# Performance work log

Hardware: AMD Instinct MI355X
Metric: run time of the kernel (lower is better)

Reference implementation:

```python
import jax, jax.numpy as jnp
import numpy as np

N = 8192        # number of nodes (adjacency is N x N)
F_IN = 256      # in_features
F_OUT = 256     # out_features


def setup_inputs() -> dict:
    key = jax.random.key(0)
    k_x, k_adj, k_kernel, k_bias, k_beta = jax.random.split(key, 5)
    x = jax.random.normal(k_x, (N, F_IN), dtype=jnp.float32)
    adj = jax.random.uniform(k_adj, (N, N), dtype=jnp.float32)  # dense non-negative adjacency buffer
    # xavier-uniform-like scale for the kernel
    limit = float(np.sqrt(6.0 / (F_IN + F_OUT)))
    kernel = jax.random.uniform(k_kernel, (F_IN, F_OUT), dtype=jnp.float32, minval=-limit, maxval=limit)
    bias = 0.01 * jax.random.normal(k_bias, (F_OUT,), dtype=jnp.float32)
    beta = 0.01 * jax.random.normal(k_beta, (N,), dtype=jnp.float32)
    return {"x": x, "adj": adj, "kernel": kernel, "bias": bias, "beta": beta}


def reference(x, adj, kernel, bias, beta):
    # Original: diag(1/(rowsum(adj)+beta)) @ (adj + diag(beta)) @ x @ kernel + bias
    # Fused form: row-scale and diagonal-add applied without materializing NxN diag matrices.
    scale = jnp.reciprocal(jnp.sum(adj, axis=1) + beta)          # [N]
    agg = adj @ x + beta[:, None] * x                             # (adj + diag(beta)) @ x  -> [N, F_IN]
    return (scale[:, None] * agg) @ kernel + bias                 # [N, F_OUT]
```

## Files before the change

kernel.cpp:

```cpp
#include <hip/hip_runtime.h>
#include <hip/hip_bf16.h>


typedef __attribute__((ext_vector_type(8))) short  short8;
typedef __attribute__((ext_vector_type(4))) float  floatx4;

#define N_NODES 8192
#define F_DIM   256

#define ASYNC16(g, l)                                                          \
  __builtin_amdgcn_global_load_lds(                                           \
      (const __attribute__((address_space(1))) void*)(g),                     \
      (__attribute__((address_space(3))) void*)(l), 16, 0, 0)

__device__ __forceinline__ unsigned short f2bf(float f) {
  unsigned u = __float_as_uint(f);
  return (unsigned short)((u + 0x7FFFu + ((u >> 16) & 1u)) >> 16);
}

__device__ __forceinline__ short8 pack_bf16x8(floatx4 a, floatx4 b) {
  short8 r;
  r[0] = (short)f2bf(a.x);
  r[1] = (short)f2bf(a.y);
  r[2] = (short)f2bf(a.z);
  r[3] = (short)f2bf(a.w);
  r[4] = (short)f2bf(b.x);
  r[5] = (short)f2bf(b.y);
  r[6] = (short)f2bf(b.z);
  r[7] = (short)f2bf(b.w);
  return r;
}

__global__ __launch_bounds__(256) void tile_bf16_kernel(
    const float* __restrict__ src, unsigned short* __restrict__ dst, int K) {
  const int Nn = F_DIM;
  int cid = blockIdx.x * 256 + threadIdx.x;
  int per_kblk = Nn * 4;
  int kblk = cid / per_kblk;
  int rem  = cid - kblk * per_kblk;
  int n16 = rem >> 6;
  int kg  = (rem >> 4) & 3;
  int nl  = rem & 15;
  int n = n16 * 16 + nl;
  int k = kblk * 32 + kg * 8;
  const float* s = src + (size_t)k * Nn + n;
  floatx4 v0, v1;
  v0.x = s[0];
  v0.y = s[(size_t)Nn];
  v0.z = s[(size_t)2 * Nn];
  v0.w = s[(size_t)3 * Nn];
  v1.x = s[(size_t)4 * Nn];
  v1.y = s[(size_t)5 * Nn];
  v1.z = s[(size_t)6 * Nn];
  v1.w = s[(size_t)7 * Nn];
  *(short8*)(dst + (size_t)cid * 8) = pack_bf16x8(v0, v1);
}

template <int KS>
__global__ __launch_bounds__(256, 2) void stage1_kernel(
    const float* __restrict__ adj, const unsigned short* __restrict__ xbt,
    float* __restrict__ part, float* __restrict__ rsp) {
  __shared__ float         At[64 * 32];
  __shared__ unsigned short Bt[32 * F_DIM];

  const int tid = threadIdx.x;
  const int w  = tid >> 6;
  const int l  = tid & 63;
  const int kq = l >> 4;
  const int ml = l & 15;
  const int m0 = blockIdx.x * 64;
  const int ks = blockIdx.y;
  const int kbeg   = ks * (N_NODES / KS);
  const int KSTEPS = (N_NODES / KS) / 32;

  const int arow = w * 16 + (l >> 3);
  const int srcg = (l & 7) ^ ((l >> 3) & 7);
  const float* agp0 = adj + (size_t)(m0 + arow) * N_NODES + kbeg + srcg * 4;
  const float* agp1 = agp0 + (size_t)8 * N_NODES;
  float* aldst0 = At + (w * 2) * 256;
  float* aldst1 = At + (w * 2 + 1) * 256;
  const unsigned short* bgp =
      xbt + (size_t)(kbeg / 32) * (32 * F_DIM) + (w * 4) * 512 + l * 8;
  unsigned short* bldst = Bt + (w * 4) * 512;

  int aoff0[4], aoff1[4], boff[4];
#pragma unroll
  for (int mf = 0; mf < 4; ++mf) {
    int m = mf * 16 + ml;
    aoff0[mf] = m * 32 + (((kq * 2)     ^ (m & 7)) * 4);
    aoff1[mf] = m * 32 + (((kq * 2 + 1) ^ (m & 7)) * 4);
  }
#pragma unroll
  for (int nf = 0; nf < 4; ++nf)
    boff[nf] = (w * 4 + nf) * 512 + kq * 128 + ml * 8;

  floatx4 acc[4][4];
  const floatx4 zf4 = {0.f, 0.f, 0.f, 0.f};
#pragma unroll
  for (int mf = 0; mf < 4; ++mf)
#pragma unroll
    for (int nf = 0; nf < 4; ++nf) acc[mf][nf] = zf4;
  float rsum[4] = {0.f, 0.f, 0.f, 0.f};

  for (int s = 0; s < KSTEPS; ++s) {
    ASYNC16(agp0, aldst0);
    ASYNC16(agp1, aldst1);
    ASYNC16(bgp,         bldst);
    ASYNC16(bgp +  512,  bldst +  512);
    ASYNC16(bgp + 1024,  bldst + 1024);
    ASYNC16(bgp + 1536,  bldst + 1536);
    agp0 += 32; agp1 += 32; bgp += 32 * F_DIM;
    __syncthreads();

    short8 af[4];
#pragma unroll
    for (int mf = 0; mf < 4; ++mf) {
      floatx4 a0 = *(const floatx4*)(At + aoff0[mf]);
      floatx4 a1 = *(const floatx4*)(At + aoff1[mf]);
      if (w == 0)
        rsum[mf] += (a0.x + a0.y + a0.z + a0.w) + (a1.x + a1.y + a1.z + a1.w);
      af[mf] = pack_bf16x8(a0, a1);
    }
#pragma unroll
    for (int nf = 0; nf < 4; ++nf) {
      short8 bv = *(const short8*)(Bt + boff[nf]);
#pragma unroll
      for (int mf = 0; mf < 4; ++mf)
        acc[mf][nf] =
            __builtin_amdgcn_mfma_f32_16x16x32_bf16(af[mf], bv, acc[mf][nf], 0, 0, 0);
    }
    __syncthreads();
  }

  float* pout = part + (size_t)ks * N_NODES * F_DIM;
#pragma unroll
  for (int mf = 0; mf < 4; ++mf)
#pragma unroll
    for (int nf = 0; nf < 4; ++nf) {
      int col = w * 64 + nf * 16 + ml;
#pragma unroll
      for (int r = 0; r < 4; ++r) {
        int row = m0 + mf * 16 + kq * 4 + r;
        pout[(size_t)row * F_DIM + col] = acc[mf][nf][r];
      }
    }

  if (w == 0) {
#pragma unroll
    for (int mf = 0; mf < 4; ++mf) {
      float v = rsum[mf];
      v += __shfl_xor(v, 16);
      v += __shfl_xor(v, 32);
      if (kq == 0) rsp[ks * N_NODES + m0 + mf * 16 + ml] = v;
    }
  }
}

template <int KS>
__global__ __launch_bounds__(256, 2) void stage2_kernel(
    const float* part, const float* __restrict__ rsp,
    const float* __restrict__ x, const float* __restrict__ beta,
    const float* __restrict__ bias, const unsigned short* __restrict__ wbt,
    float* out) {
  __shared__ unsigned short At[32 * 32];
  __shared__ unsigned short Bt[32 * F_DIM];
  __shared__ float sscale[32];
  __shared__ float sbeta[32];

  const int tid = threadIdx.x;
  const int w  = tid >> 6;
  const int l  = tid & 63;
  const int kq = l >> 4;
  const int ml = l & 15;
  const int m0 = blockIdx.x * 32;

  if (tid < 32) {
    float rs = 0.f;
#pragma unroll
    for (int p = 0; p < KS; ++p) rs += rsp[p * N_NODES + m0 + tid];
    float b = beta[m0 + tid];
    sbeta[tid]  = b;
    sscale[tid] = 1.0f / (rs + b);
  }
  __syncthreads();

  floatx4 acc[2][4];
  const floatx4 zf4 = {0.f, 0.f, 0.f, 0.f};
#pragma unroll
  for (int mf = 0; mf < 2; ++mf)
#pragma unroll
    for (int nf = 0; nf < 4; ++nf) acc[mf][nf] = zf4;

  const unsigned short* bgp = wbt + (w * 4) * 512 + l * 8;
  unsigned short* bldst = Bt + (w * 4) * 512;

  for (int s = 0; s < 8; ++s) {
    ASYNC16(bgp,        bldst);
    ASYNC16(bgp +  512, bldst +  512);
    ASYNC16(bgp + 1024, bldst + 1024);
    ASYNC16(bgp + 1536, bldst + 1536);
    bgp += 32 * F_DIM;

    if (tid < 128) {
      int r = tid >> 2, g = tid & 3;
      size_t off = (size_t)(m0 + r) * F_DIM + s * 32 + g * 8;
      floatx4 v0 = *(const floatx4*)(x + off);
      floatx4 v1 = *(const floatx4*)(x + off + 4);
      float bb = sbeta[r];
      v0 *= bb; v1 *= bb;
#pragma unroll
      for (int p = 0; p < KS; ++p) {
        const float* pp = part + (size_t)p * N_NODES * F_DIM + off;
        v0 += *(const floatx4*)pp;
        v1 += *(const floatx4*)(pp + 4);
      }
      float sc = sscale[r];
      v0 *= sc; v1 *= sc;
      *(short8*)(At + r * 32 + ((g ^ (r & 3)) * 8)) = pack_bf16x8(v0, v1);
    }
    __syncthreads();

    short8 af[2];
#pragma unroll
    for (int mf = 0; mf < 2; ++mf) {
      int m = mf * 16 + ml;
      af[mf] = *(const short8*)(At + m * 32 + ((kq ^ (m & 3)) * 8));
    }
#pragma unroll
    for (int nf = 0; nf < 4; ++nf) {
      short8 bv = *(const short8*)(Bt + (w * 4 + nf) * 512 + kq * 128 + ml * 8);
#pragma unroll
      for (int mf = 0; mf < 2; ++mf)
        acc[mf][nf] =
            __builtin_amdgcn_mfma_f32_16x16x32_bf16(af[mf], bv, acc[mf][nf], 0, 0, 0);
    }
    __syncthreads();
  }

#pragma unroll
  for (int nf = 0; nf < 4; ++nf) {
    int col = w * 64 + nf * 16 + ml;
    float bv = bias[col];
#pragma unroll
    for (int mf = 0; mf < 2; ++mf)
#pragma unroll
      for (int r = 0; r < 4; ++r) {
        int row = m0 + mf * 16 + kq * 4 + r;
        out[(size_t)row * F_DIM + col] = acc[mf][nf][r] + bv;
      }
  }
}

extern "C" void kernel_launch(void* const* d_in, const int* in_sizes, int n_in,
                              void* d_out, int out_size, void* d_ws, size_t ws_size,
                              hipStream_t stream) {
  const float* x    = (const float*)d_in[0];
  const float* adj  = (const float*)d_in[1];
  const float* kern = (const float*)d_in[2];
  const float* bias = (const float*)d_in[3];
  const float* beta = (const float*)d_in[4];
  float* out = (float*)d_out;

  char* ws = (char*)d_ws;
  unsigned short* xbt = (unsigned short*)ws;
  unsigned short* wbt = xbt + (size_t)N_NODES * F_DIM;
  float* rsp  = (float*)(wbt + F_DIM * F_DIM);
  float* part = (float*)((char*)rsp + 4 * N_NODES * sizeof(float));

  const size_t base    = (size_t)N_NODES * F_DIM * 2 + (size_t)F_DIM * F_DIM * 2 +
                         4 * (size_t)N_NODES * 4;
  const size_t part_sz = (size_t)N_NODES * F_DIM * 4;

  tile_bf16_kernel<<<(N_NODES * F_DIM / 8) / 256, 256, 0, stream>>>(x, xbt, N_NODES);
  tile_bf16_kernel<<<(F_DIM * F_DIM / 8) / 256, 256, 0, stream>>>(kern, wbt, F_DIM);

  if (ws_size >= base + 4 * part_sz) {
    stage1_kernel<4><<<dim3(128, 4), 256, 0, stream>>>(adj, xbt, part, rsp);
    stage2_kernel<4><<<256, 256, 0, stream>>>(part, rsp, x, beta, bias, wbt, out);
  } else if (ws_size >= base + 2 * part_sz) {
    stage1_kernel<2><<<dim3(128, 2), 256, 0, stream>>>(adj, xbt, part, rsp);
    stage2_kernel<2><<<256, 256, 0, stream>>>(part, rsp, x, beta, bias, wbt, out);
  } else {
    stage1_kernel<1><<<dim3(128, 1), 256, 0, stream>>>(adj, xbt, out, rsp);
    stage2_kernel<1><<<256, 256, 0, stream>>>(out, rsp, x, beta, bias, wbt, out);
  }
}
```

Before: 431.9 us.

## Fuse both GEMM stages into one kernel with a 3-stage async LDS pipeline

Replaces the split-K stage1 and the separate stage2 kernel with one fused kernel. Each 512-thread block owns 32 rows and loops over the full K. A triple-buffered global_load_lds pipeline waits on vmcnt, with BK=64. The aggregated tile is scaled, given the beta*x term, converted to bf16 in LDS and multiplied by the kernel weights in the same block. This removes the fp32 partial-sum round trip through global memory and one launch, and overlaps loads with MFMA. In exchange it uses about 123KB of LDS per block (likely one block per CU), has no split-K parallelism, and re-reads xbt once per row tile.

Result: faster. 416.9 us (-3.5%).

```diff
diff --git a/kernel.cpp b/kernel.cpp
--- a/kernel.cpp
+++ b/kernel.cpp
@@ -7,6 +7,8 @@
 
 #define N_NODES 8192
 #define F_DIM   256
+#define BK      64
+#define NSTEPS  (N_NODES / BK)
 
 #define ASYNC16(g, l)                                                          \
   __builtin_amdgcn_global_load_lds(                                           \
@@ -56,198 +58,155 @@
   *(short8*)(dst + (size_t)cid * 8) = pack_bf16x8(v0, v1);
 }
 
-template <int KS>
-__global__ __launch_bounds__(256, 2) void stage1_kernel(
+__global__ __launch_bounds__(512, 2) void fused_kernel(
     const float* __restrict__ adj, const unsigned short* __restrict__ xbt,
-    float* __restrict__ part, float* __restrict__ rsp) {
-  __shared__ float         At[64 * 32];
-  __shared__ unsigned short Bt[32 * F_DIM];
-
-  const int tid = threadIdx.x;
-  const int w  = tid >> 6;
-  const int l  = tid & 63;
-  const int kq = l >> 4;
-  const int ml = l & 15;
-  const int m0 = blockIdx.x * 64;
-  const int ks = blockIdx.y;
-  const int kbeg   = ks * (N_NODES / KS);
-  const int KSTEPS = (N_NODES / KS) / 32;
-
-  const int arow = w * 16 + (l >> 3);
-  const int srcg = (l & 7) ^ ((l >> 3) & 7);
-  const float* agp0 = adj + (size_t)(m0 + arow) * N_NODES + kbeg + srcg * 4;
-  const float* agp1 = agp0 + (size_t)8 * N_NODES;
-  float* aldst0 = At + (w * 2) * 256;
-  float* aldst1 = At + (w * 2 + 1) * 256;
-  const unsigned short* bgp =
-      xbt + (size_t)(kbeg / 32) * (32 * F_DIM) + (w * 4) * 512 + l * 8;
-  unsigned short* bldst = Bt + (w * 4) * 512;
-
-  int aoff0[4], aoff1[4], boff[4];
-#pragma unroll
-  for (int mf = 0; mf < 4; ++mf) {
-    int m = mf * 16 + ml;
-    aoff0[mf] = m * 32 + (((kq * 2)     ^ (m & 7)) * 4);
-    aoff1[mf] = m * 32 + (((kq * 2 + 1) ^ (m & 7)) * 4);
-  }
-#pragma unroll
-  for (int nf = 0; nf < 4; ++nf)
-    boff[nf] = (w * 4 + nf) * 512 + kq * 128 + ml * 8;
-
-  floatx4 acc[4][4];
-  const floatx4 zf4 = {0.f, 0.f, 0.f, 0.f};
-#pragma unroll
-  for (int mf = 0; mf < 4; ++mf)
-#pragma unroll
-    for (int nf = 0; nf < 4; ++nf) acc[mf][nf] = zf4;
-  float rsum[4] = {0.f, 0.f, 0.f, 0.f};
-
-  for (int s = 0; s < KSTEPS; ++s) {
-    ASYNC16(agp0, aldst0);
-    ASYNC16(agp1, aldst1);
-    ASYNC16(bgp,         bldst);
-    ASYNC16(bgp +  512,  bldst +  512);
-    ASYNC16(bgp + 1024,  bldst + 1024);
-    ASYNC16(bgp + 1536,  bldst + 1536);
-    agp0 += 32; agp1 += 32; bgp += 32 * F_DIM;
-    __syncthreads();
-
-    short8 af[4];
-#pragma unroll
-    for (int mf = 0; mf < 4; ++mf) {
-      floatx4 a0 = *(const floatx4*)(At + aoff0[mf]);
-      floatx4 a1 = *(const floatx4*)(At + aoff1[mf]);
-      if (w == 0)
-        rsum[mf] += (a0.x + a0.y + a0.z + a0.w) + (a1.x + a1.y + a1.z + a1.w);
-      af[mf] = pack_bf16x8(a0, a1);
-    }
-#pragma unroll
-    for (int nf = 0; nf < 4; ++nf) {
-      short8 bv = *(const short8*)(Bt + boff[nf]);
-#pragma unroll
-      for (int mf = 0; mf < 4; ++mf)
-        acc[mf][nf] =
-            __builtin_amdgcn_mfma_f32_16x16x32_bf16(af[mf], bv, acc[mf][nf], 0, 0, 0);
-    }
-    __syncthreads();
-  }
-
-  float* pout = part + (size_t)ks * N_NODES * F_DIM;
-#pragma unroll
-  for (int mf = 0; mf < 4; ++mf)
-#pragma unroll
-    for (int nf = 0; nf < 4; ++nf) {
-      int col = w * 64 + nf * 16 + ml;
-#pragma unroll
-      for (int r = 0; r < 4; ++r) {
-        int row = m0 + mf * 16 + kq * 4 + r;
-        pout[(size_t)row * F_DIM + col] = acc[mf][nf][r];
-      }
-    }
-
-  if (w == 0) {
-#pragma unroll
-    for (int mf = 0; mf < 4; ++mf) {
-      float v = rsum[mf];
-      v += __shfl_xor(v, 16);
-      v += __shfl_xor(v, 32);
-      if (kq == 0) rsp[ks * N_NODES + m0 + mf * 16 + ml] = v;
-    }
-  }
-}
-
-template <int KS>
-__global__ __launch_bounds__(256, 2) void stage2_kernel(
-    const float* part, const float* __restrict__ rsp,
     const float* __restrict__ x, const float* __restrict__ beta,
     const float* __restrict__ bias, const unsigned short* __restrict__ wbt,
-    float* out) {
-  __shared__ unsigned short At[32 * 32];
-  __shared__ unsigned short Bt[32 * F_DIM];
-  __shared__ float sscale[32];
-  __shared__ float sbeta[32];
+    float* __restrict__ out) {
+  __shared__ __attribute__((aligned(16))) char smem[123136];
+  float* sscale = (float*)(smem + 122880);
+  float* sbeta  = (float*)(smem + 123008);
 
   const int tid = threadIdx.x;
-  const int w  = tid >> 6;
-  const int l  = tid & 63;
-  const int kq = l >> 4;
-  const int ml = l & 15;
-  const int m0 = blockIdx.x * 32;
-
-  if (tid < 32) {
-    float rs = 0.f;
-#pragma unroll
-    for (int p = 0; p < KS; ++p) rs += rsp[p * N_NODES + m0 + tid];
-    float b = beta[m0 + tid];
-    sbeta[tid]  = b;
-    sscale[tid] = 1.0f / (rs + b);
-  }
+  const int w   = tid >> 6;
+  const int l   = tid & 63;
+  const int kq  = l >> 4;
+  const int ml  = l & 15;
+  const int wm  = w >> 2;
+  const int wn  = w & 3;
+  const int m0  = blockIdx.x * 32;
+
+  const int arow = tid >> 4;
+  const int agrp = tid & 15;
+  const float* asrc_base =
+      adj + (size_t)(m0 + arow) * N_NODES + ((agrp ^ (arow & 7)) << 2);
+  const unsigned short* bsrc_base = xbt + (size_t)tid * 8;
+
+  const int frow = wm * 16 + ml;
+  int aoff[2][2];
+#pragma unroll
+  for (int kb = 0; kb < 2; ++kb) {
+    int g0 = kb * 8 + kq * 2;
+    aoff[kb][0] = frow * 64 + (((g0)     ^ (frow & 7)) << 2);
+    aoff[kb][1] = frow * 64 + (((g0 + 1) ^ (frow & 7)) << 2);
+  }
+  const int boffbase = wn * 2048 + kq * 128 + ml * 8;
+
+  floatx4 acc[4];
+  const floatx4 zf4 = {0.f, 0.f, 0.f, 0.f};
+#pragma unroll
+  for (int nf = 0; nf < 4; ++nf) acc[nf] = zf4;
+  float rsum = 0.f;
+
+#pragma unroll
+  for (int s = 0; s < 2; ++s) {
+    ASYNC16(asrc_base + s * BK, smem + s * 8192 + (w << 10));
+    const unsigned short* bs = bsrc_base + (size_t)s * 16384;
+    char* bd = smem + 24576 + s * 32768 + (w << 10);
+#pragma unroll
+    for (int q = 0; q < 4; ++q) ASYNC16(bs + q * 4096, bd + q * 8192);
+  }
+
+  auto compute = [&](int cur) {
+    const float* Af = (const float*)(smem + cur * 8192);
+    const unsigned short* Bf = (const unsigned short*)(smem + 24576 + cur * 32768);
+    short8 af[2];
+#pragma unroll
+    for (int kb = 0; kb < 2; ++kb) {
+      floatx4 a0 = *(const floatx4*)(Af + aoff[kb][0]);
+      floatx4 a1 = *(const floatx4*)(Af + aoff[kb][1]);
+      if (wn == 0)
+        rsum += (a0.x + a0.y + a0.z + a0.w) + (a1.x + a1.y + a1.z + a1.w);
+      af[kb] = pack_bf16x8(a0, a1);
+    }
+#pragma unroll
+    for (int nf = 0; nf < 4; ++nf) {
+      short8 b0 = *(const short8*)(Bf + boffbase + nf * 512);
+      short8 b1 = *(const short8*)(Bf + 8192 + boffbase + nf * 512);
+      acc[nf] = __builtin_amdgcn_mfma_f32_16x16x32_bf16(af[0], b0, acc[nf], 0, 0, 0);
+      acc[nf] = __builtin_amdgcn_mfma_f32_16x16x32_bf16(af[1], b1, acc[nf], 0, 0, 0);
+    }
+  };
+
+  int cur = 0, stg = 2;
+  for (int s = 0; s < NSTEPS - 2; ++s) {
+    asm volatile("s_waitcnt vmcnt(5)\n\ts_barrier" ::: "memory");
+    ASYNC16(asrc_base + (s + 2) * BK, smem + stg * 8192 + (w << 10));
+    {
+      const unsigned short* bs = bsrc_base + (size_t)(s + 2) * 16384;
+      char* bd = smem + 24576 + stg * 32768 + (w << 10);
+#pragma unroll
+      for (int q = 0; q < 4; ++q) ASYNC16(bs + q * 4096, bd + q * 8192);
+    }
+    compute(cur);
+    cur = cur + 1; if (cur == 3) cur = 0;
+    stg = stg + 1; if (stg == 3) stg = 0;
+  }
+  for (int s = NSTEPS - 2; s < NSTEPS; ++s) {
+    asm volatile("s_waitcnt vmcnt(0)\n\ts_barrier" ::: "memory");
+    compute(cur);
+    cur = cur + 1; if (cur == 3) cur = 0;
+  }
+
   __syncthreads();
 
-  floatx4 acc[2][4];
-  const floatx4 zf4 = {0.f, 0.f, 0.f, 0.f};
-#pragma unroll
-  for (int mf = 0; mf < 2; ++mf)
-#pragma unroll
-    for (int nf = 0; nf < 4; ++nf) acc[mf][nf] = zf4;
-
-  const unsigned short* bgp = wbt + (w * 4) * 512 + l * 8;
-  unsigned short* bldst = Bt + (w * 4) * 512;
-
-  for (int s = 0; s < 8; ++s) {
-    ASYNC16(bgp,        bldst);
-    ASYNC16(bgp +  512, bldst +  512);
-    ASYNC16(bgp + 1024, bldst + 1024);
-    ASYNC16(bgp + 1536, bldst + 1536);
-    bgp += 32 * F_DIM;
-
-    if (tid < 128) {
-      int r = tid >> 2, g = tid & 3;
-      size_t off = (size_t)(m0 + r) * F_DIM + s * 32 + g * 8;
-      floatx4 v0 = *(const floatx4*)(x + off);
-      floatx4 v1 = *(const floatx4*)(x + off + 4);
-      float bb = sbeta[r];
-      v0 *= bb; v1 *= bb;
-#pragma unroll
-      for (int p = 0; p < KS; ++p) {
-        const float* pp = part + (size_t)p * N_NODES * F_DIM + off;
-        v0 += *(const floatx4*)pp;
-        v1 += *(const floatx4*)(pp + 4);
-      }
-      float sc = sscale[r];
-      v0 *= sc; v1 *= sc;
-      *(short8*)(At + r * 32 + ((g ^ (r & 3)) * 8)) = pack_bf16x8(v0, v1);
-    }
-    __syncthreads();
-
-    short8 af[2];
-#pragma unroll
-    for (int mf = 0; mf < 2; ++mf) {
-      int m = mf * 16 + ml;
-      af[mf] = *(const short8*)(At + m * 32 + ((kq ^ (m & 3)) * 8));
-    }
+  {
+    const float* xs = x + (size_t)m0 * F_DIM + tid * 4;
+    char* xd = smem + 24576 + (w << 10);
+#pragma unroll
+    for (int q = 0; q < 4; ++q) ASYNC16(xs + q * 2048, xd + q * 8192);
+  }
+  if (wn == 0) {
+    float rs = rsum;
+    rs += __shfl_xor(rs, 16);
+    rs += __shfl_xor(rs, 32);
+    if (l < 16) {
+      float b = beta[m0 + wm * 16 + l];
+      sbeta[wm * 16 + l]  = b;
+      sscale[wm * 16 + l] = 1.0f / (rs + b);
+    }
+  }
+  __syncthreads();
+
+  const float* xl = (const float*)(smem + 24576);
+  unsigned short* G = (unsigned short*)smem;
+#pragma unroll
+  for (int nf = 0; nf < 4; ++nf) {
+    int col = wn * 64 + nf * 16 + ml;
+    int chunk = col >> 3;
+#pragma unroll
+    for (int r = 0; r < 4; ++r) {
+      int row = wm * 16 + kq * 4 + r;
+      float g = sscale[row] * (acc[nf][r] + sbeta[row] * xl[row * F_DIM + col]);
+      G[row * 256 + (((chunk ^ (row & 7)) << 3) | (col & 7))] = f2bf(g);
+    }
+  }
+  __syncthreads();
+
+  floatx4 acc2[4];
+#pragma unroll
+  for (int nf = 0; nf < 4; ++nf) acc2[nf] = zf4;
+  const int grow = wm * 16 + ml;
+#pragma unroll
+  for (int s2 = 0; s2 < 8; ++s2) {
+    short8 ag = *(const short8*)(G + grow * 256 +
+                                 (((s2 * 4 + kq) ^ (grow & 7)) << 3));
+    const unsigned short* wb = wbt + s2 * 8192 + boffbase;
 #pragma unroll
     for (int nf = 0; nf < 4; ++nf) {
-      short8 bv = *(const short8*)(Bt + (w * 4 + nf) * 512 + kq * 128 + ml * 8);
-#pragma unroll
-      for (int mf = 0; mf < 2; ++mf)
-        acc[mf][nf] =
-            __builtin_amdgcn_mfma_f32_16x16x32_bf16(af[mf], bv, acc[mf][nf], 0, 0, 0);
-    }
-    __syncthreads();
-  }
-
+      short8 bv = *(const short8*)(wb + nf * 512);
+      acc2[nf] = __builtin_amdgcn_mfma_f32_16x16x32_bf16(ag, bv, acc2[nf], 0, 0, 0);
+    }
+  }
 #pragma unroll
   for (int nf = 0; nf < 4; ++nf) {
-    int col = w * 64 + nf * 16 + ml;
+    int col = wn * 64 + nf * 16 + ml;
     float bv = bias[col];
 #pragma unroll
-    for (int mf = 0; mf < 2; ++mf)
-#pragma unroll
-      for (int r = 0; r < 4; ++r) {
-        int row = m0 + mf * 16 + kq * 4 + r;
-        out[(size_t)row * F_DIM + col] = acc[mf][nf][r] + bv;
-      }
+    for (int r = 0; r < 4; ++r) {
+      int row = m0 + wm * 16 + kq * 4 + r;
+      out[(size_t)row * F_DIM + col] = acc2[nf][r] + bv;
+    }
   }
 }
 
@@ -264,24 +223,8 @@
   char* ws = (char*)d_ws;
   unsigned short* xbt = (unsigned short*)ws;
   unsigned short* wbt = xbt + (size_t)N_NODES * F_DIM;
-  float* rsp  = (float*)(wbt + F_DIM * F_DIM);
-  float* part = (float*)((char*)rsp + 4 * N_NODES * sizeof(float));
-
-  const size_t base    = (size_t)N_NODES * F_DIM * 2 + (size_t)F_DIM * F_DIM * 2 +
-                         4 * (size_t)N_NODES * 4;
-  const size_t part_sz = (size_t)N_NODES * F_DIM * 4;
 
   tile_bf16_kernel<<<(N_NODES * F_DIM / 8) / 256, 256, 0, stream>>>(x, xbt, N_NODES);
   tile_bf16_kernel<<<(F_DIM * F_DIM / 8) / 256, 256, 0, stream>>>(kern, wbt, F_DIM);
-
-  if (ws_size >= base + 4 * part_sz) {
-    stage1_kernel<4><<<dim3(128, 4), 256, 0, stream>>>(adj, xbt, part, rsp);
-    stage2_kernel<4><<<256, 256, 0, stream>>>(part, rsp, x, beta, bias, wbt, out);
-  } else if (ws_size >= base + 2 * part_sz) {
-    stage1_kernel<2><<<dim3(128, 2), 256, 0, stream>>>(adj, xbt, part, rsp);
-    stage2_kernel<2><<<256, 256, 0, stream>>>(part, rsp, x, beta, bias, wbt, out);
-  } else {
-    stage1_kernel<1><<<dim3(128, 1), 256, 0, stream>>>(adj, xbt, out, rsp);
-    stage2_kernel<1><<<256, 256, 0, stream>>>(out, rsp, x, beta, bias, wbt, out);
-  }
-}
+  fused_kernel<<<256, 512, 0, stream>>>(adj, xbt, x, beta, bias, wbt, out);
+}
```

## Triple-buffer stage1 LDS loads with async prefetch two steps ahead

Applied to the files above, without the earlier changes.

Replaces the single-buffered load-then-compute loop in stage1 with a three-slot LDS ring. Async global-to-LDS copies are issued two k-steps ahead, and each step uses one explicit waitcnt plus barrier instead of two __syncthreads. This is meant to hide adj/x load latency behind MFMA work. It raises LDS use to 72KB per block, which may limit the two-blocks-per-CU target, and drops the KS=2 fallback path.

Measured after the change: 432.6 us. No clear change (+0.2%).

```diff
diff --git a/kernel.cpp b/kernel.cpp
--- a/kernel.cpp
+++ b/kernel.cpp
@@ -56,12 +56,54 @@
   *(short8*)(dst + (size_t)cid * 8) = pack_bf16x8(v0, v1);
 }
 
+#define MFMA16(a, b, c) __builtin_amdgcn_mfma_f32_16x16x32_bf16(a, b, c, 0, 0, 0)
+
+#define STAGE(s, c)                                                            \
+  {                                                                            \
+    ASYNC16(agp0 + (size_t)(s) * 32, smem + (c) * 8192 + (w * 2) * 1024);      \
+    ASYNC16(agp1 + (size_t)(s) * 32, smem + (c) * 8192 + (w * 2 + 1) * 1024);  \
+    const unsigned short* bs_ = bgp + (size_t)(s) * 8192;                      \
+    char* bd_ = smem + 24576 + (c) * 16384 + (w * 4) * 1024;                   \
+    ASYNC16(bs_,        bd_);                                                  \
+    ASYNC16(bs_ +  512, bd_ + 1024);                                           \
+    ASYNC16(bs_ + 1024, bd_ + 2048);                                           \
+    ASYNC16(bs_ + 1536, bd_ + 3072);                                           \
+  }
+
+#define COMPUTE(c)                                                             \
+  {                                                                            \
+    const float* At_ = (const float*)(smem + (c) * 8192);                      \
+    const unsigned short* Bt_ =                                                \
+        (const unsigned short*)(smem + 24576 + (c) * 16384);                   \
+    short8 af[4];                                                              \
+    _Pragma("unroll") for (int mf = 0; mf < 4; ++mf) {                         \
+      floatx4 a0 = *(const floatx4*)(At_ + aoff0[mf]);                         \
+      floatx4 a1 = *(const floatx4*)(At_ + aoff1[mf]);                         \
+      if (w == 0)       \
+        rsum[mf] += (a0.x + a0.y + a0.z + a0.w) + (a1.x + a1.y + a1.z + a1.w); \
+      af[mf] = pack_bf16x8(a0, a1);                                            \
+    }                                                                          \
+    _Pragma("unroll") for (int nf = 0; nf < 4; ++nf) {                         \
+      short8 bv = *(const short8*)(Bt_ + boff[nf]);                            \
+      _Pragma("unroll") for (int mf = 0; mf < 4; ++mf)                         \
+        acc[mf][nf] = MFMA16(af[mf], bv, acc[mf][nf]);                         \
+    }                                                                          \
+  }
+
+#define ITER(s, c, cn)                                                         \
+  asm volatile("s_waitcnt vmcnt(6) lgkmcnt(0)\n\ts_barrier" ::: "memory");     \
+  STAGE((s) + 2, cn);                                                          \
+  COMPUTE(c);
+
 template <int KS>
 __global__ __launch_bounds__(256, 2) void stage1_kernel(
     const float* __restrict__ adj, const unsigned short* __restrict__ xbt,
     float* __restrict__ part, float* __restrict__ rsp) {
-  __shared__ float         At[64 * 32];
-  __shared__ unsigned short Bt[32 * F_DIM];
+  constexpr int KSTEPS = (N_NODES / KS) / 32;
+  constexpr int TMAIN  = (KSTEPS - 4) / 3;
+  static_assert(TMAIN * 3 + 4 == KSTEPS, "KSTEPS-4 must be divisible by 3");
+
+  __shared__ __attribute__((aligned(16))) char smem[73728];
 
   const int tid = threadIdx.x;
   const int w  = tid >> 6;
@@ -70,18 +112,14 @@
   const int ml = l & 15;
   const int m0 = blockIdx.x * 64;
   const int ks = blockIdx.y;
-  const int kbeg   = ks * (N_NODES / KS);
-  const int KSTEPS = (N_NODES / KS) / 32;
+  const int kbeg = ks * (N_NODES / KS);
 
   const int arow = w * 16 + (l >> 3);
   const int srcg = (l & 7) ^ ((l >> 3) & 7);
   const float* agp0 = adj + (size_t)(m0 + arow) * N_NODES + kbeg + srcg * 4;
   const float* agp1 = agp0 + (size_t)8 * N_NODES;
-  float* aldst0 = At + (w * 2) * 256;
-  float* aldst1 = At + (w * 2 + 1) * 256;
   const unsigned short* bgp =
       xbt + (size_t)(kbeg / 32) * (32 * F_DIM) + (w * 4) * 512 + l * 8;
-  unsigned short* bldst = Bt + (w * 4) * 512;
 
   int aoff0[4], aoff1[4], boff[4];
 #pragma unroll
@@ -102,35 +140,21 @@
     for (int nf = 0; nf < 4; ++nf) acc[mf][nf] = zf4;
   float rsum[4] = {0.f, 0.f, 0.f, 0.f};
 
-  for (int s = 0; s < KSTEPS; ++s) {
-    ASYNC16(agp0, aldst0);
-    ASYNC16(agp1, aldst1);
-    ASYNC16(bgp,         bldst);
-    ASYNC16(bgp +  512,  bldst +  512);
-    ASYNC16(bgp + 1024,  bldst + 1024);
-    ASYNC16(bgp + 1536,  bldst + 1536);
-    agp0 += 32; agp1 += 32; bgp += 32 * F_DIM;
-    __syncthreads();
-
-    short8 af[4];
-#pragma unroll
-    for (int mf = 0; mf < 4; ++mf) {
-      floatx4 a0 = *(const floatx4*)(At + aoff0[mf]);
-      floatx4 a1 = *(const floatx4*)(At + aoff1[mf]);
-      if (w == 0)
-        rsum[mf] += (a0.x + a0.y + a0.z + a0.w) + (a1.x + a1.y + a1.z + a1.w);
-      af[mf] = pack_bf16x8(a0, a1);
-    }
-#pragma unroll
-    for (int nf = 0; nf < 4; ++nf) {
-      short8 bv = *(const short8*)(Bt + boff[nf]);
-#pragma unroll
-      for (int mf = 0; mf < 4; ++mf)
-        acc[mf][nf] =
-            __builtin_amdgcn_mfma_f32_16x16x32_bf16(af[mf], bv, acc[mf][nf], 0, 0, 0);
-    }
-    __syncthreads();
-  }
+  STAGE(0, 0);
+  STAGE(1, 1);
+
+  for (int t = 0; t < TMAIN; ++t) {
+    const int s0 = 3 * t;
+    ITER(s0,     0, 2);
+    ITER(s0 + 1, 1, 0);
+    ITER(s0 + 2, 2, 1);
+  }
+  ITER(KSTEPS - 4, 0, 2);
+  ITER(KSTEPS - 3, 1, 0);
+  asm volatile("s_waitcnt vmcnt(6) lgkmcnt(0)\n\ts_barrier" ::: "memory");
+  COMPUTE(2);
+  asm volatile("s_waitcnt vmcnt(0) lgkmcnt(0)\n\ts_barrier" ::: "memory");
+  COMPUTE(0);
 
   float* pout = part + (size_t)ks * N_NODES * F_DIM;
 #pragma unroll
@@ -155,6 +179,10 @@
     }
   }
 }
+
+#undef ITER
+#undef COMPUTE
+#undef STAGE
 
 template <int KS>
 __global__ __launch_bounds__(256, 2) void stage2_kernel(
@@ -231,8 +259,7 @@
       short8 bv = *(const short8*)(Bt + (w * 4 + nf) * 512 + kq * 128 + ml * 8);
 #pragma unroll
       for (int mf = 0; mf < 2; ++mf)
-        acc[mf][nf] =
-            __builtin_amdgcn_mfma_f32_16x16x32_bf16(af[mf], bv, acc[mf][nf], 0, 0, 0);
+        acc[mf][nf] = MFMA16(af[mf], bv, acc[mf][nf]);
     }
     __syncthreads();
   }
@@ -277,9 +304,6 @@
   if (ws_size >= base + 4 * part_sz) {
     stage1_kernel<4><<<dim3(128, 4), 256, 0, stream>>>(adj, xbt, part, rsp);
     stage2_kernel<4><<<256, 256, 0, stream>>>(part, rsp, x, beta, bias, wbt, out);
-  } else if (ws_size >= base + 2 * part_sz) {
-    stage1_kernel<2><<<dim3(128, 2), 256, 0, stream>>>(adj, xbt, part, rsp);
-    stage2_kernel<2><<<256, 256, 0, stream>>>(part, rsp, x, beta, bias, wbt, out);
   } else {
     stage1_kernel<1><<<dim3(128, 1), 256, 0, stream>>>(adj, xbt, out, rsp);
     stage2_kernel<1><<<256, 256, 0, stream>>>(out, rsp, x, beta, bias, wbt, out);
```
